# Kernel tuning notes

Hardware: AMD Instinct MI355X
Metric: run time of the kernel (lower is better)

The kernel has to match this reference:

```python
import jax, jax.numpy as jnp
import numpy as np

T = 16384  # total training steps (length of LR schedule)
M = 8192   # number of evaluated checkpoints
HUBER_DELTA = 0.001


def _huber(delta, r):
    a = jnp.abs(r)
    return jnp.where(a <= delta, 0.5 * r * r, delta * (a - 0.5 * delta))


def setup_inputs() -> dict:
    key = jax.random.key(0)
    k1, k2, k3 = jax.random.split(key, 3)
    # realistic positive LR schedule (~3e-4), required since lrs**(-gamma) is taken
    lrs = jax.random.uniform(k1, (T,), dtype=jnp.float32) * 3e-4 + 1e-5
    lr_sum = jnp.cumsum(lrs)
    step = jnp.sort(jax.random.randint(k2, (M,), 0, T))
    S1 = lr_sum[step]  # cumulative LR sum at the evaluated steps
    # lr_gap = consecutive LR differences (delta of the schedule); index 0 unused
    lr_gap = jnp.concatenate([jnp.zeros((1,), jnp.float32), lrs[:-1] - lrs[1:]])
    loss = jax.random.uniform(k3, (M,), dtype=jnp.float32) + 2.0  # positive (log taken)
    p = lambda v: jnp.float32(v)
    return {
        "S1": S1, "lrs": lrs, "lr_sum": lr_sum, "step": step,
        "lr_gap": lr_gap, "loss": loss,
        "L0": p(2.5), "A": p(0.5), "alpha": p(0.5), "B": p(300.0),
        "C": p(1.0), "beta": p(0.5), "gamma": p(0.6),
    }


def reference(S1, lrs, lr_sum, step, lr_gap, loss, L0, A, alpha, B, C, beta, gamma):
    # Vectorized triangular reduction replacing the per-step Python loop:
    # for step s: LD = sum_{k=1..s} lr_gap[k] * (1 - (1 + C*lrs[k]^-gamma*(lr_sum[s]-lr_sum[k-1]))^-beta)
    Tn = lrs.shape[0]
    k = jnp.arange(Tn)
    mask = (k[None, :] >= 1) & (k[None, :] <= step[:, None])  # [M, T]
    lr_sum_prev = jnp.concatenate([jnp.zeros((1,), lr_sum.dtype), lr_sum[:-1]])
    G = lr_sum[step][:, None] - lr_sum_prev[None, :]          # lr_sum[s] - lr_sum[k-1]
    G = jnp.where(mask, G, 0.0)                               # keep base positive where masked
    inner = 1.0 + C * (lrs ** (-gamma))[None, :] * G          # [M, T]
    term = lr_gap[None, :] * (1.0 - inner ** (-beta))
    LD = jnp.sum(jnp.where(mask, term, 0.0), axis=1)          # [M]
    pred = L0 + A * S1 ** (-alpha) + B * LD
    r = jnp.log(loss) - jnp.log(jnp.clip(pred, 1e-10))
    return _huber(HUBER_DELTA, r).sum()
```

## Files before the change

kernel.cpp:

```cpp
#include <hip/hip_runtime.h>
#include <math.h>

#define BLK 512
#define GSZ 8
#define SEGW 128
#define NSEG_NEAR 6
#define NDEG 8
#define SEGSTRIDE 16

#if __has_builtin(__builtin_amdgcn_rsqf)
#define RSQF(x) __builtin_amdgcn_rsqf(x)
#else
#define RSQF(x) (1.0f / sqrtf(x))
#endif
#if __has_builtin(__builtin_amdgcn_rcpf)
#define RCPF(x) __builtin_amdgcn_rcpf(x)
#else
#define RCPF(x) (1.0f / (x))
#endif

__device__ __forceinline__ float fast_pow(float x, float e) {
  return __expf(e * __logf(x));
}

__global__ __launch_bounds__(256) void precompute_kernel(
    const float* __restrict__ lrs, const float* __restrict__ lr_sum,
    const float* __restrict__ lr_gap,
    float* __restrict__ cpw, float* __restrict__ dd, float* __restrict__ gapp,
    float* __restrict__ dk, float* __restrict__ wk,
    const float* __restrict__ gamma_p, const float* __restrict__ C_p,
    const float* __restrict__ beta_p, int T, int Tpad) {
  int i = blockIdx.x * 256 + threadIdx.x;
  if (i >= Tpad) return;
  if (i == 0 || i >= T) {
    cpw[i] = 0.0f; dd[i] = 1.0f; gapp[i] = 0.0f; dk[i] = 0.0f; wk[i] = 0.0f;
    return;
  }
  float g = lr_gap[i];
  float L = lr_sum[i - 1];
  float c = C_p[0] * fast_pow(lrs[i], -gamma_p[0]);
  cpw[i]  = c;
  dd[i]   = fmaf(-c, L, 1.0f);
  gapp[i] = g;
  dk[i]   = 1.0f / c - L;
  wk[i]   = g * fast_pow(c, -beta_p[0]);
}

__global__ __launch_bounds__(128) void moments_kernel(
    const float* __restrict__ dk, const float* __restrict__ wk,
    float* __restrict__ segdata, const float* __restrict__ beta_p) {
  int seg = blockIdx.x, t = threadIdx.x;
  int k = seg * SEGW + t;
  float d = dk[k], w = wk[k];
  __shared__ float sh[2];

  float v = d;
#pragma unroll
  for (int off = 32; off; off >>= 1) v += __shfl_down(v, off, 64);
  if ((t & 63) == 0) sh[t >> 6] = v;
  __syncthreads();
  float d0 = (sh[0] + sh[1]) * (1.0f / 128.0f);
  __syncthreads();

  float delta = d - d0;
  float p = w;
  float beta = beta_p[0];
  float b = 1.0f;
  for (int n = 0; n <= NDEG; ++n) {
    v = p;
#pragma unroll
    for (int off = 32; off; off >>= 1) v += __shfl_down(v, off, 64);
    if ((t & 63) == 0) sh[t >> 6] = v;
    __syncthreads();
    if (t == 0) segdata[seg * SEGSTRIDE + 1 + n] = b * (sh[0] + sh[1]);
    __syncthreads();
    p *= delta;
    b *= (-beta - (float)n) / (float)(n + 1);
  }
  if (t == 0) segdata[seg * SEGSTRIDE] = d0;
}

template <bool USE_RSQ>
__device__ __forceinline__ void body(
    const float* __restrict__ cpw, const float* __restrict__ dd,
    const float* __restrict__ gapp, const float* __restrict__ segdata,
    const float (&Ss)[GSZ], const int (&sv)[GSZ], const int (&kseg)[GSZ],
    float (&acc)[GSZ], int nsegmax, int base, int smaxb, float nb, int tid) {
  for (int seg = tid; seg < nsegmax; seg += BLK) {
    const float* sd = segdata + seg * SEGSTRIDE;
    float d0 = sd[0];
    float m[NDEG + 1];
#pragma unroll
    for (int n = 0; n <= NDEG; ++n) m[n] = sd[1 + n];
#pragma unroll
    for (int j = 0; j < GSZ; ++j) {
      float s_ = Ss[j] + d0;
      float r = RCPF(s_);
      float tb = USE_RSQ ? RSQF(s_) : fast_pow(s_, nb);
      float h = m[NDEG];
#pragma unroll
      for (int n = NDEG - 1; n >= 0; --n) h = fmaf(h, r, m[n]);
      float contrib = tb * h;
      acc[j] += (seg < kseg[j]) ? contrib : 0.0f;
    }
  }

  for (int kb = base + tid * 4; kb <= smaxb; kb += BLK * 4) {
    float4 c4 = *(const float4*)(cpw + kb);
    float4 d4 = *(const float4*)(dd + kb);
    float4 g4 = *(const float4*)(gapp + kb);
    const float ce[4] = {c4.x, c4.y, c4.z, c4.w};
    const float de[4] = {d4.x, d4.y, d4.z, d4.w};
    const float ge[4] = {g4.x, g4.y, g4.z, g4.w};
#pragma unroll
    for (int e = 0; e < 4; ++e) {
#pragma unroll
      for (int j = 0; j < GSZ; ++j) {
        float inner = fmaf(ce[e], Ss[j], de[e]);
        float p = USE_RSQ ? RSQF(inner) : __expf(nb * __logf(inner));
        int kk = kb + e;
        float pm = (kk >= (kseg[j] << 7) && kk <= sv[j]) ? p : 0.0f;
        acc[j] = fmaf(ge[e], pm, acc[j]);
      }
    }
  }
}

__global__ __launch_bounds__(BLK, 4) void ld_kernel(
    const float* __restrict__ S1, const int* __restrict__ step,
    const float* __restrict__ loss, const float* __restrict__ lrs,
    const float* __restrict__ cpw, const float* __restrict__ dd,
    const float* __restrict__ gapp, const float* __restrict__ segdata,
    const float* __restrict__ L0_p, const float* __restrict__ A_p,
    const float* __restrict__ alpha_p, const float* __restrict__ B_p,
    const float* __restrict__ beta_p,
    float* __restrict__ hub) {
  __shared__ float wacc[BLK / 64][GSZ];
  int tid = threadIdx.x;
  int mbase = blockIdx.x * GSZ;

  float Ss[GSZ]; int sv[GSZ]; int kseg[GSZ]; float acc[GSZ];
#pragma unroll
  for (int j = 0; j < GSZ; ++j) {
    Ss[j] = S1[mbase + j];
    sv[j] = step[mbase + j];
    kseg[j] = max(0, (sv[j] >> 7) - NSEG_NEAR);
    acc[j] = 0.0f;
  }
  int ksegmin = kseg[0], nsegmax = kseg[0], smaxb = sv[0];
#pragma unroll
  for (int j = 1; j < GSZ; ++j) {
    ksegmin = min(ksegmin, kseg[j]);
    nsegmax = max(nsegmax, kseg[j]);
    smaxb = max(smaxb, sv[j]);
  }
  int base = ksegmin << 7;

  float beta = beta_p[0];
  float nb = -beta;
  if (beta == 0.5f)
    body<true>(cpw, dd, gapp, segdata, Ss, sv, kseg, acc,
               nsegmax, base, smaxb, nb, tid);
  else
    body<false>(cpw, dd, gapp, segdata, Ss, sv, kseg, acc,
                nsegmax, base, smaxb, nb, tid);

  int lane = tid & 63, wid = tid >> 6;
#pragma unroll
  for (int j = 0; j < GSZ; ++j) {
    float v = acc[j];
#pragma unroll
    for (int off = 32; off; off >>= 1) v += __shfl_down(v, off, 64);
    if (lane == 0) wacc[wid][j] = v;
  }
  __syncthreads();

  if (tid < GSZ) {
    int j = tid;
    int m = mbase + j;
    float sgp = 0.0f;
#pragma unroll
    for (int w = 0; w < BLK / 64; ++w) sgp += wacc[w][j];
    int s = step[m];
    float Ssum = S1[m];
    float LD = (lrs[0] - lrs[s]) - sgp;
    float pred = L0_p[0] + A_p[0] * fast_pow(Ssum, -alpha_p[0]) + B_p[0] * LD;
    pred = fmaxf(pred, 1e-10f);
    float r = __logf(loss[m]) - __logf(pred);
    float a = fabsf(r);
    const float dlt = 0.001f;
    hub[m] = (a <= dlt) ? (0.5f * r * r) : (dlt * (a - 0.5f * dlt));
  }
}

__global__ __launch_bounds__(1024) void reduce_kernel(
    const float* __restrict__ hub, float* __restrict__ out, int M) {
  float acc = 0.0f;
  for (int i = threadIdx.x; i < M; i += 1024) acc += hub[i];
#pragma unroll
  for (int off = 32; off; off >>= 1) acc += __shfl_down(acc, off, 64);
  __shared__ float wacc[16];
  int lane = threadIdx.x & 63, wid = threadIdx.x >> 6;
  if (lane == 0) wacc[wid] = acc;
  __syncthreads();
  if (threadIdx.x == 0) {
    float t = 0.0f;
#pragma unroll
    for (int i = 0; i < 16; ++i) t += wacc[i];
    out[0] = t;
  }
}

extern "C" void kernel_launch(void* const* d_in, const int* in_sizes, int n_in,
                              void* d_out, int out_size, void* d_ws, size_t ws_size,
                              hipStream_t stream) {
  const float* S1      = (const float*)d_in[0];
  const float* lrs     = (const float*)d_in[1];
  const float* lr_sum  = (const float*)d_in[2];
  const int*   step    = (const int*)  d_in[3];
  const float* lr_gap  = (const float*)d_in[4];
  const float* loss    = (const float*)d_in[5];
  const float* L0_p    = (const float*)d_in[6];
  const float* A_p     = (const float*)d_in[7];
  const float* alpha_p = (const float*)d_in[8];
  const float* B_p     = (const float*)d_in[9];
  const float* C_p     = (const float*)d_in[10];
  const float* beta_p  = (const float*)d_in[11];
  const float* gamma_p = (const float*)d_in[12];

  int M = in_sizes[0];
  int T = in_sizes[1];
  int Tpad = ((T + 2047) / 2048) * 2048;
  int nseg = Tpad / SEGW;

  float* cpw  = (float*)d_ws;
  float* dd   = cpw + Tpad;
  float* gapp = dd + Tpad;
  float* dk   = gapp + Tpad;
  float* wk   = dk + Tpad;
  float* segd = wk + Tpad;
  float* hub  = segd + nseg * SEGSTRIDE;

  precompute_kernel<<<(Tpad + 255) / 256, 256, 0, stream>>>(
      lrs, lr_sum, lr_gap, cpw, dd, gapp, dk, wk,
      gamma_p, C_p, beta_p, T, Tpad);
  moments_kernel<<<nseg, 128, 0, stream>>>(dk, wk, segd, beta_p);
  ld_kernel<<<M / GSZ, BLK, 0, stream>>>(
      S1, step, loss, lrs, cpw, dd, gapp, segd,
      L0_p, A_p, alpha_p, B_p, beta_p, hub);
  reduce_kernel<<<1, 1024, 0, stream>>>(hub, (float*)d_out, M);
}
```

Baseline: 26.42 us.

## Fuse precompute and segment-moment kernels and simplify the LD inner-loop masking

Merges the per-element precompute kernel and the per-segment moments kernel into one prep kernel, so the d/w intermediates stay in registers instead of being written to and re-read from workspace. This also removes one kernel launch. The far-segment loop in ld_kernel becomes a single guarded pass, which assumes the segment count never exceeds the block size. The near-range mask becomes a single unsigned compare on precomputed lo/range values, and the non-0.5 beta path moves into a noinline function to ease register pressure on the hot path. Padding is reduced to one extra segment, and the fused kernel assumes T is a multiple of the segment width, since early-returning threads sit before a __syncthreads.

```diff
diff --git a/kernel.cpp b/kernel.cpp
--- a/kernel.cpp
+++ b/kernel.cpp
@@ -23,38 +23,35 @@
   return __expf(e * __logf(x));
 }
 
-__global__ __launch_bounds__(256) void precompute_kernel(
+__global__ __launch_bounds__(128) void prep_kernel(
     const float* __restrict__ lrs, const float* __restrict__ lr_sum,
     const float* __restrict__ lr_gap,
     float* __restrict__ cpw, float* __restrict__ dd, float* __restrict__ gapp,
-    float* __restrict__ dk, float* __restrict__ wk,
+    float* __restrict__ segdata,
     const float* __restrict__ gamma_p, const float* __restrict__ C_p,
-    const float* __restrict__ beta_p, int T, int Tpad) {
-  int i = blockIdx.x * 256 + threadIdx.x;
-  if (i >= Tpad) return;
-  if (i == 0 || i >= T) {
-    cpw[i] = 0.0f; dd[i] = 1.0f; gapp[i] = 0.0f; dk[i] = 0.0f; wk[i] = 0.0f;
-    return;
-  }
-  float g = lr_gap[i];
-  float L = lr_sum[i - 1];
-  float c = C_p[0] * fast_pow(lrs[i], -gamma_p[0]);
-  cpw[i]  = c;
-  dd[i]   = fmaf(-c, L, 1.0f);
-  gapp[i] = g;
-  dk[i]   = 1.0f / c - L;
-  wk[i]   = g * fast_pow(c, -beta_p[0]);
-}
-
-__global__ __launch_bounds__(128) void moments_kernel(
-    const float* __restrict__ dk, const float* __restrict__ wk,
-    float* __restrict__ segdata, const float* __restrict__ beta_p) {
+    const float* __restrict__ beta_p, int T) {
   int seg = blockIdx.x, t = threadIdx.x;
   int k = seg * SEGW + t;
-  float d = dk[k], w = wk[k];
+  if (k >= T) {
+    cpw[k] = 0.0f; dd[k] = 1.0f; gapp[k] = 0.0f;
+    return;
+  }
+  float d_ = 0.0f, w_ = 0.0f;
+  if (k == 0) {
+    cpw[0] = 0.0f; dd[0] = 1.0f; gapp[0] = 0.0f;
+  } else {
+    float g = lr_gap[k];
+    float L = lr_sum[k - 1];
+    float c = C_p[0] * fast_pow(lrs[k], -gamma_p[0]);
+    cpw[k]  = c;
+    dd[k]   = fmaf(-c, L, 1.0f);
+    gapp[k] = g;
+    d_ = 1.0f / c - L;
+    w_ = g * fast_pow(c, -beta_p[0]);
+  }
+
   __shared__ float sh[2];
-
-  float v = d;
+  float v = d_;
 #pragma unroll
   for (int off = 32; off; off >>= 1) v += __shfl_down(v, off, 64);
   if ((t & 63) == 0) sh[t >> 6] = v;
@@ -62,8 +59,8 @@
   float d0 = (sh[0] + sh[1]) * (1.0f / 128.0f);
   __syncthreads();
 
-  float delta = d - d0;
-  float p = w;
+  float delta = d_ - d0;
+  float p = w_;
   float beta = beta_p[0];
   float b = 1.0f;
   for (int n = 0; n <= NDEG; ++n) {
@@ -81,13 +78,13 @@
 }
 
 template <bool USE_RSQ>
-__device__ __forceinline__ void body(
+__device__ __forceinline__ void body2(
     const float* __restrict__ cpw, const float* __restrict__ dd,
     const float* __restrict__ gapp, const float* __restrict__ segdata,
-    const float (&Ss)[GSZ], const int (&sv)[GSZ], const int (&kseg)[GSZ],
+    const float (&Ss)[GSZ], const int (&lo)[GSZ], const int (&rng)[GSZ],
     float (&acc)[GSZ], int nsegmax, int base, int smaxb, float nb, int tid) {
-  for (int seg = tid; seg < nsegmax; seg += BLK) {
-    const float* sd = segdata + seg * SEGSTRIDE;
+  if (tid < nsegmax) {
+    const float* sd = segdata + tid * SEGSTRIDE;
     float d0 = sd[0];
     float m[NDEG + 1];
 #pragma unroll
@@ -101,10 +98,9 @@
 #pragma unroll
       for (int n = NDEG - 1; n >= 0; --n) h = fmaf(h, r, m[n]);
       float contrib = tb * h;
-      acc[j] += (seg < kseg[j]) ? contrib : 0.0f;
+      acc[j] += (tid < (lo[j] >> 7)) ? contrib : 0.0f;
     }
   }
-
   for (int kb = base + tid * 4; kb <= smaxb; kb += BLK * 4) {
     float4 c4 = *(const float4*)(cpw + kb);
     float4 d4 = *(const float4*)(dd + kb);
@@ -118,12 +114,21 @@
       for (int j = 0; j < GSZ; ++j) {
         float inner = fmaf(ce[e], Ss[j], de[e]);
         float p = USE_RSQ ? RSQF(inner) : __expf(nb * __logf(inner));
-        int kk = kb + e;
-        float pm = (kk >= (kseg[j] << 7) && kk <= sv[j]) ? p : 0.0f;
+        unsigned off = (unsigned)(kb + e - lo[j]);
+        float pm = (off <= (unsigned)rng[j]) ? p : 0.0f;
         acc[j] = fmaf(ge[e], pm, acc[j]);
       }
     }
   }
+}
+
+__device__ __attribute__((noinline)) void cold_body(
+    const float* cpw, const float* dd, const float* gapp,
+    const float* segdata, const float (&Ss)[GSZ], const int (&lo)[GSZ],
+    const int (&rng)[GSZ], float (&acc)[GSZ], int nsegmax, int base,
+    int smaxb, float nb, int tid) {
+  body2<false>(cpw, dd, gapp, segdata, Ss, lo, rng, acc,
+               nsegmax, base, smaxb, nb, tid);
 }
 
 __global__ __launch_bounds__(BLK, 4) void ld_kernel(
@@ -139,31 +144,29 @@
   int tid = threadIdx.x;
   int mbase = blockIdx.x * GSZ;
 
-  float Ss[GSZ]; int sv[GSZ]; int kseg[GSZ]; float acc[GSZ];
+  float Ss[GSZ]; int lo[GSZ]; int rng[GSZ]; float acc[GSZ];
+  int nsegmax = 0, base = 1 << 30, smaxb = 0;
 #pragma unroll
   for (int j = 0; j < GSZ; ++j) {
     Ss[j] = S1[mbase + j];
-    sv[j] = step[mbase + j];
-    kseg[j] = max(0, (sv[j] >> 7) - NSEG_NEAR);
+    int s = step[mbase + j];
+    int ks = max(0, (s >> 7) - NSEG_NEAR);
+    lo[j] = ks << 7;
+    rng[j] = s - lo[j];
     acc[j] = 0.0f;
-  }
-  int ksegmin = kseg[0], nsegmax = kseg[0], smaxb = sv[0];
-#pragma unroll
-  for (int j = 1; j < GSZ; ++j) {
-    ksegmin = min(ksegmin, kseg[j]);
-    nsegmax = max(nsegmax, kseg[j]);
-    smaxb = max(smaxb, sv[j]);
-  }
-  int base = ksegmin << 7;
+    nsegmax = max(nsegmax, ks);
+    base = min(base, lo[j]);
+    smaxb = max(smaxb, s);
+  }
 
   float beta = beta_p[0];
   float nb = -beta;
   if (beta == 0.5f)
-    body<true>(cpw, dd, gapp, segdata, Ss, sv, kseg, acc,
-               nsegmax, base, smaxb, nb, tid);
+    body2<true>(cpw, dd, gapp, segdata, Ss, lo, rng, acc,
+                nsegmax, base, smaxb, nb, tid);
   else
-    body<false>(cpw, dd, gapp, segdata, Ss, sv, kseg, acc,
-                nsegmax, base, smaxb, nb, tid);
+    cold_body(cpw, dd, gapp, segdata, Ss, lo, rng, acc,
+              nsegmax, base, smaxb, nb, tid);
 
   int lane = tid & 63, wid = tid >> 6;
 #pragma unroll
@@ -230,21 +233,18 @@
 
   int M = in_sizes[0];
   int T = in_sizes[1];
-  int Tpad = ((T + 2047) / 2048) * 2048;
-  int nseg = Tpad / SEGW;
+  int Tpad = T + SEGW;
+  int nseg_launch = Tpad / SEGW;
 
   float* cpw  = (float*)d_ws;
   float* dd   = cpw + Tpad;
   float* gapp = dd + Tpad;
-  float* dk   = gapp + Tpad;
-  float* wk   = dk + Tpad;
-  float* segd = wk + Tpad;
-  float* hub  = segd + nseg * SEGSTRIDE;
-
-  precompute_kernel<<<(Tpad + 255) / 256, 256, 0, stream>>>(
-      lrs, lr_sum, lr_gap, cpw, dd, gapp, dk, wk,
-      gamma_p, C_p, beta_p, T, Tpad);
-  moments_kernel<<<nseg, 128, 0, stream>>>(dk, wk, segd, beta_p);
+  float* segd = gapp + Tpad;
+  float* hub  = segd + 128 * SEGSTRIDE;
+
+  prep_kernel<<<nseg_launch, 128, 0, stream>>>(
+      lrs, lr_sum, lr_gap, cpw, dd, gapp, segd,
+      gamma_p, C_p, beta_p, T);
   ld_kernel<<<M / GSZ, BLK, 0, stream>>>(
       S1, step, loss, lrs, cpw, dd, gapp, segd,
       L0_p, A_p, alpha_p, B_p, beta_p, hub);
```

New measurement: 35.02 us. 32.6% more time.
